# Kernel optimization log

Hardware: AMD Instinct MI355X
Metric: run time of the kernel (lower is better)

## Reference

```python
import jax, jax.numpy as jnp
import numpy as np

NUM_SLOTS = 50
NUM_TAGS = 1 + 2 * NUM_SLOTS  # 'O' + B-/I- per slot = 101
BATCH = 256
SEQ_LEN = 2048


def _build_type_indices():
    # Replicates CRF.build_transitions index construction for a BIO label vocab.
    labels = ['O'] + [p + f's{i}' for i in range(NUM_SLOTS) for p in ('B-', 'I-')]
    m1 = {'O': 0, 'B': 1, 'I': 2}
    m2 = {'O': 0, 'B': 3, 'I': 4}
    t0 = np.zeros((NUM_TAGS, NUM_TAGS), dtype=np.int64)
    t1 = np.zeros((NUM_TAGS, NUM_TAGS), dtype=np.int64)
    for i, li in enumerate(labels):
        for j, lj in enumerate(labels):
            if li != 'O' and li[2:] != lj[2:]:
                t0[i, j], t1[i, j] = m1[li[0]], m2[lj[0]]
            else:
                t0[i, j], t1[i, j] = m1[li[0]], m1[lj[0]]
    return jnp.asarray(t0), jnp.asarray(t1)


def setup_inputs() -> dict:
    key = jax.random.key(0)
    k1, k2, k3, k4, k5, k6 = jax.random.split(key, 6)
    feats = jax.random.normal(k1, (BATCH, SEQ_LEN, NUM_TAGS), dtype=jnp.float32)
    # cdt_transitions is log of the fixed prior table in the original module
    cdt = jnp.log(jnp.array([[0.6, 0.4, 0.001, 0.001, 0.001],
                             [0.3, 0.1, 0.1, 0.5, 0.001],
                             [0.6, 0.1, 0.1, 0.2, 0.001]], dtype=jnp.float32))
    start_transitions = jax.random.normal(k2, (NUM_TAGS,), dtype=jnp.float32)
    stop_transitions = jax.random.normal(k3, (NUM_TAGS,), dtype=jnp.float32)
    # random valid lengths in [S/2, S]; mask[:, :len] = 1
    lengths = jax.random.randint(k4, (BATCH,), SEQ_LEN // 2, SEQ_LEN + 1)
    mask = (jnp.arange(SEQ_LEN)[None, :] < lengths[:, None]).astype(jnp.int32)
    tags = jax.random.randint(k5, (BATCH, SEQ_LEN), 0, NUM_TAGS)
    types0, types1 = _build_type_indices()
    return {
        'feats': feats,
        'cdt_transitions': cdt,
        'start_transitions': start_transitions,
        'stop_transitions': stop_transitions,
        'mask': mask,
        'tags': tags,
        'types0': types0,
        'types1': types1,
    }


def reference(feats, cdt_transitions, start_transitions, stop_transitions,
              mask, tags, types0, types1):
    # build_transitions: gather (num_tags, num_tags) log-transition matrix
    trans = cdt_transitions[types0, types1]  # (T, T)
    B, S, T = feats.shape
    maskb = mask.astype(bool)

    # ---- forward algorithm (log partition) via lax.scan over time ----
    feats_t = jnp.swapaxes(feats, 0, 1)   # (S, B, T)
    mask_t = jnp.swapaxes(maskb, 0, 1)    # (S, B)
    partition0 = feats_t[0] + start_transitions[None, :]  # (B, T)

    def step(partition, xs):
        f, mk = xs  # f: (B, T), mk: (B,)
        # cur_values[b, i, j] = f[b, j] + partition[b, i] + trans[i, j]
        cur = f[:, None, :] + partition[:, :, None] + trans[None, :, :]
        cur_partition = jax.nn.logsumexp(cur, axis=1)  # (B, T)
        new_partition = jnp.where(mk[:, None], cur_partition, partition)
        return new_partition, None

    partition, _ = jax.lax.scan(step, partition0, (feats_t[1:], mask_t[1:]))
    forward_score = jax.nn.logsumexp(partition + stop_transitions[None, :], axis=1)  # (B,)

    # ---- gold path score ----
    mf = maskb.astype(feats.dtype)
    feat_score = jnp.sum(
        jnp.take_along_axis(feats, tags[..., None], axis=2)[..., 0] * mf, axis=1)
    trans_score = jnp.sum(trans[tags[:, :-1], tags[:, 1:]] * mf[:, 1:], axis=1)
    start_score = start_transitions[tags[:, 0]]
    lengths = jnp.sum(mask, axis=1).astype(jnp.int32)  # (B,)
    end_ids = jnp.take_along_axis(tags, (lengths - 1)[:, None], axis=1)[:, 0]
    stop_score = stop_transitions[end_ids]
    gold_score = feat_score + start_score + trans_score + stop_score

    return forward_score - gold_score  # (B,) negative log-likelihood per sequence
```

## Files before the change

kernel.cpp:

```cpp
#include <hip/hip_runtime.h>
#include <math.h>

#define NSLOTS 50
#define T 101
#define SEQ 2048
#define CHUNK 16

template<int CTRL>
__device__ __forceinline__ float dpp_xadd(float v) {
    int x = __builtin_amdgcn_update_dpp(0, __float_as_int(v), CTRL, 0xF, 0xF, true);
    return v + __int_as_float(x);
}

__device__ __forceinline__ float wsum64(float v) {
    v = dpp_xadd<0xB1>(v);
    v = dpp_xadd<0x4E>(v);
    v = dpp_xadd<0x141>(v);
    v = dpp_xadd<0x140>(v);
    v = dpp_xadd<0x142>(v);
    v = dpp_xadd<0x143>(v);
    int s = __builtin_amdgcn_readlane(__float_as_int(v), 63);
    return __int_as_float(s);
}

__device__ __forceinline__ void gl_lds(const float* g, float* lds) {
#if __has_builtin(__builtin_amdgcn_global_load_lds)
    __builtin_amdgcn_global_load_lds((const __attribute__((address_space(1))) void*)g,
        (__attribute__((address_space(3))) void*)lds, 4, 0, 0);
#else
    lds[threadIdx.x & 63] = *g;
#endif
}

__device__ __forceinline__ float frcp(float x) {
#if __has_builtin(__builtin_amdgcn_rcpf)
    return __builtin_amdgcn_rcpf(x);
#else
    return 1.0f / x;
#endif
}
__device__ __forceinline__ float flog2(float x) {
#if __has_builtin(__builtin_amdgcn_log2f)
    return __builtin_amdgcn_log2f(x);
#else
    return log2f(x);
#endif
}

__global__ __launch_bounds__(128, 1) void crf_nll_kernel(
    const float* __restrict__ feats,
    const float* __restrict__ cdt,
    const float* __restrict__ start_t,
    const float* __restrict__ stop_t,
    const int*   __restrict__ mask,
    const int*   __restrict__ tags,
    float*       __restrict__ out)
{
    const int b = blockIdx.x, tid = threadIdx.x;
    const int wave = tid >> 6, l = tid & 63;
    const float* fb = feats + (size_t)b * SEQ * T;
    const int*   mb = mask + (size_t)b * SEQ;
    const int*   tb = tags + (size_t)b * SEQ;

    __shared__ float S[64 * 128];
    __shared__ float res[2];

    float mc = 0.f;
    for (int t = l; t < SEQ; t += 64) mc += (float)mb[t];
    const int len    = (int)(wsum64(mc) + 0.5f);
    const int nsteps = len - 1;
    const int nper   = (nsteps + CHUNK - 1) / CHUNK;
    const int nfull  = nsteps / CHUNK;

    const float actm = (l < NSLOTS) ? 1.f : 0.f;
    const int aB = (2*l+1 <= 100) ? 2*l+1 : 100;
    const int aI = (2*l+2 <= 100) ? 2*l+2 : 100;
    const int s1 = (2*l+1 <= 100) ? 2*l+1 : 0;
    const int s2 = (2*l+2 <= 100) ? 2*l+2 : 0;

    float L[15];
    #pragma unroll
    for (int i = 0; i < 15; ++i) L[i] = cdt[i];
    const float pOO=__expf(L[0]),  pOB=__expf(L[1]),  pOI=__expf(L[2]);
    const float pBO=__expf(L[5]),  pBBs=__expf(L[6]), pBIs=__expf(L[7]),
                pBBd=__expf(L[8]), pBId=__expf(L[9]);
    const float pIO=__expf(L[10]), pIBs=__expf(L[11]), pIIs=__expf(L[12]),
                pIBd=__expf(L[13]), pIId=__expf(L[14]);
    const float dBB=pBBs-pBBd, dIB=pIBs-pIBd, dBI=pBIs-pBId, dII=pIIs-pIId;

    float eB=0.f, eI=0.f, accF=0.f, accL2=0.f;
    float f0B=0,f0I=0,f0O=0,f1B=0,f1I=0,f1O=0;
    float gs = 0.f;

    if (wave == 1) {
        #pragma unroll
        for (int k = 0; k < 2*CHUNK; ++k) {
            const float* row = fb + (size_t)(1 + k) * T;
            float* dst = &S[(size_t)k * 128];
            gl_lds(row + s1, dst);
            gl_lds(row + s2, dst + 64);
        }
    } else {
        float pO0 = fb[0] + start_t[0];
        eB = actm * __expf(fb[aB] + start_t[aB] - pO0);
        eI = actm * __expf(fb[aI] + start_t[aI] - pO0);
        accF = pO0;
    }
    __syncthreads();

    if (wave == 0) {
        f0B = S[l];       f0I = S[64 + l];       f0O = S[50];
        f1B = S[128 + l]; f1I = S[128 + 64 + l]; f1O = S[128 + 50];
    }

#define STEP_BODY(GUARDED)                                                    \
    {                                                                         \
        const int t  = 1 + p * CHUNK + k;                                     \
        const int w2 = ((t + 1) & 63) << 7;     \
        float nB = S[w2 + l], nI = S[w2 + 64 + l], nO = S[w2 + 50];           \
        if (!(GUARDED) || t <= nsteps) {                                      \
            float gB = actm * __expf(f0B - f0O);               \
            float gI = actm * __expf(f0I - f0O);                              \
            float SBs = wsum64(eB);                                           \
            float SIs = wsum64(eI);                                           \
            float uB = __builtin_fmaf(eB,dBB,__builtin_fmaf(eI,dIB,pOB));     \
            float uI = __builtin_fmaf(eB,dBI,__builtin_fmaf(eI,dII,pOI));     \
            float zB = __builtin_fmaf(SIs,pIBd,__builtin_fmaf(SBs,pBBd,uB));  \
            float zI = __builtin_fmaf(SIs,pIId,__builtin_fmaf(SBs,pBId,uI));  \
            float zO = __builtin_fmaf(SIs,pIO, __builtin_fmaf(SBs,pBO,pOO));  \
            float rz = frcp(zO);                                              \
            eB = (gB * zB) * rz;                                              \
            eI = (gI * zI) * rz;                                              \
            accL2 += flog2(zO);                                \
            accF  += f0O;                                      \
        }                                                                     \
        f0B=f1B; f0I=f1I; f0O=f1O; f1B=nB; f1I=nI; f1O=nO;                    \
    }

    for (int p = 0; p < nper; ++p) {
        if (wave == 0) {
            if (p < nfull) {
                #pragma unroll
                for (int k = 0; k < CHUNK; ++k) STEP_BODY(false)
            } else {
                #pragma unroll
                for (int k = 0; k < CHUNK; ++k) STEP_BODY(true)
            }
        } else {
            const int ci = p + 2;
            #pragma unroll
            for (int k = 0; k < CHUNK; ++k) {
                int t = 1 + ci * CHUNK + k;
                t = (t < SEQ) ? t : (SEQ - 1);
                const float* row = fb + (size_t)t * T;
                float* dst = &S[(size_t)((ci * CHUNK + k) & 63) * 128];
                gl_lds(row + s1, dst);
                gl_lds(row + s2, dst + 64);
            }
            if (p < (SEQ / 64)) {
                int t0 = (p << 6) + l;
                if (t0 < len) {
                    int tg = tb[t0];
                    gs += fb[(size_t)t0 * T + tg];
                    if (t0 >= 1) {
                        int i  = tb[t0 - 1];
                        int c1 = (i == 0) ? 0 : ((i & 1) ? 1 : 2);
                        int c2 = (tg == 0) ? 0 : ((tg & 1) ? 1 : 2);
                        int si = (i - 1) >> 1, sj = (tg - 1) >> 1;
                        int t1 = (i != 0 && si != sj) ? ((c2 == 0) ? 0 : c2 + 2) : c2;
                        gs += cdt[c1 * 5 + t1];
                    }
                }
            }
        }
        __syncthreads();
    }
#undef STEP_BODY

    if (wave == 0) {
        float wsum = actm * (eB * __expf(stop_t[aB]) + eI * __expf(stop_t[aI]));
        float tot  = wsum64(wsum) + __expf(stop_t[0]);
        float fwd  = accF + 0.69314718055994530942f * accL2 + __logf(tot);
        if (l == 0) res[0] = fwd;
    } else {
        float gold = wsum64(gs);
        if (l == 0) res[1] = gold + start_t[tb[0]] + stop_t[tb[len - 1]];
    }
    __syncthreads();
    if (tid == 0) out[b] = res[0] - res[1];
}

extern "C" void kernel_launch(void* const* d_in, const int* in_sizes, int n_in,
                              void* d_out, int out_size, void* d_ws, size_t ws_size,
                              hipStream_t stream) {
    const float* feats   = (const float*)d_in[0];
    const float* cdt     = (const float*)d_in[1];
    const float* start_t = (const float*)d_in[2];
    const float* stop_t  = (const float*)d_in[3];
    const int*   mask    = (const int*)d_in[4];
    const int*   tags    = (const int*)d_in[5];
    float* out = (float*)d_out;

    crf_nll_kernel<<<256, 128, 0, stream>>>(feats, cdt, start_t, stop_t, mask, tags, out);
}
```

Measured before the change: 266.9 us.

## Use unnormalized O-state with exponent-only rescaling and add gold-score wave

The forward recurrence now keeps an unnormalized O-state scale xO and renormalizes by a power of two taken from its exponent bits. This removes the per-step reciprocal and log2 from the serial critical path, and the uB/uI partial sums are precomputed for the next step. A third wave computes the gold-path score by reading feature values already staged in LDS instead of issuing separate global gathers, which takes that work off the prefetch wave. The cost is a larger block and extra LDS reads, plus the numerical risk that comes from power-of-two scaling.

```diff
diff --git a/kernel.cpp b/kernel.cpp
--- a/kernel.cpp
+++ b/kernel.cpp
@@ -32,22 +32,7 @@
 #endif
 }
 
-__device__ __forceinline__ float frcp(float x) {
-#if __has_builtin(__builtin_amdgcn_rcpf)
-    return __builtin_amdgcn_rcpf(x);
-#else
-    return 1.0f / x;
-#endif
-}
-__device__ __forceinline__ float flog2(float x) {
-#if __has_builtin(__builtin_amdgcn_log2f)
-    return __builtin_amdgcn_log2f(x);
-#else
-    return log2f(x);
-#endif
-}
-
-__global__ __launch_bounds__(128, 1) void crf_nll_kernel(
+__global__ __launch_bounds__(192, 1) void crf_nll_kernel(
     const float* __restrict__ feats,
     const float* __restrict__ cdt,
     const float* __restrict__ start_t,
@@ -78,17 +63,15 @@
     const int s1 = (2*l+1 <= 100) ? 2*l+1 : 0;
     const int s2 = (2*l+2 <= 100) ? 2*l+2 : 0;
 
-    float L[15];
-    #pragma unroll
-    for (int i = 0; i < 15; ++i) L[i] = cdt[i];
-    const float pOO=__expf(L[0]),  pOB=__expf(L[1]),  pOI=__expf(L[2]);
-    const float pBO=__expf(L[5]),  pBBs=__expf(L[6]), pBIs=__expf(L[7]),
-                pBBd=__expf(L[8]), pBId=__expf(L[9]);
-    const float pIO=__expf(L[10]), pIBs=__expf(L[11]), pIIs=__expf(L[12]),
-                pIBd=__expf(L[13]), pIId=__expf(L[14]);
+    const float pOO=__expf(cdt[0]),  pOB=__expf(cdt[1]),  pOI=__expf(cdt[2]);
+    const float pBO=__expf(cdt[5]),  pBBs=__expf(cdt[6]), pBIs=__expf(cdt[7]),
+                pBBd=__expf(cdt[8]), pBId=__expf(cdt[9]);
+    const float pIO=__expf(cdt[10]), pIBs=__expf(cdt[11]), pIIs=__expf(cdt[12]),
+                pIBd=__expf(cdt[13]), pIId=__expf(cdt[14]);
     const float dBB=pBBs-pBBd, dIB=pIBs-pIBd, dBI=pBIs-pBId, dII=pIIs-pIId;
 
-    float eB=0.f, eI=0.f, accF=0.f, accL2=0.f;
+    float xB=0.f, xI=0.f, xO=1.f, accF=0.f, uB=0.f, uI=0.f, pOOxO=pOO;
+    int accE = 0;
     float f0B=0,f0I=0,f0O=0,f1B=0,f1I=0,f1O=0;
     float gs = 0.f;
 
@@ -100,11 +83,18 @@
             gl_lds(row + s1, dst);
             gl_lds(row + s2, dst + 64);
         }
+    } else if (wave == 0) {
+        float pO0 = fb[0] + start_t[0];
+        xB = actm * __expf(fb[aB] + start_t[aB] - pO0);
+        xI = actm * __expf(fb[aI] + start_t[aI] - pO0);
+        accF = pO0;
+        uB = __builtin_fmaf(xB, dBB, __builtin_fmaf(xI, dIB, pOB));
+        uI = __builtin_fmaf(xB, dBI, __builtin_fmaf(xI, dII, pOI));
     } else {
-        float pO0 = fb[0] + start_t[0];
-        eB = actm * __expf(fb[aB] + start_t[aB] - pO0);
-        eI = actm * __expf(fb[aI] + start_t[aI] - pO0);
-        accF = pO0;
+        if (l == 0) {
+            int tg0 = tb[0];
+            gs = fb[tg0] + start_t[tg0];
+        }
     }
     __syncthreads();
 
@@ -113,28 +103,29 @@
         f1B = S[128 + l]; f1I = S[128 + 64 + l]; f1O = S[128 + 50];
     }
 
-#define STEP_BODY(GUARDED)                                                    \
-    {                                                                         \
-        const int t  = 1 + p * CHUNK + k;                                     \
-        const int w2 = ((t + 1) & 63) << 7;     \
-        float nB = S[w2 + l], nI = S[w2 + 64 + l], nO = S[w2 + 50];           \
-        if (!(GUARDED) || t <= nsteps) {                                      \
-            float gB = actm * __expf(f0B - f0O);               \
-            float gI = actm * __expf(f0I - f0O);                              \
-            float SBs = wsum64(eB);                                           \
-            float SIs = wsum64(eI);                                           \
-            float uB = __builtin_fmaf(eB,dBB,__builtin_fmaf(eI,dIB,pOB));     \
-            float uI = __builtin_fmaf(eB,dBI,__builtin_fmaf(eI,dII,pOI));     \
-            float zB = __builtin_fmaf(SIs,pIBd,__builtin_fmaf(SBs,pBBd,uB));  \
-            float zI = __builtin_fmaf(SIs,pIId,__builtin_fmaf(SBs,pBId,uI));  \
-            float zO = __builtin_fmaf(SIs,pIO, __builtin_fmaf(SBs,pBO,pOO));  \
-            float rz = frcp(zO);                                              \
-            eB = (gB * zB) * rz;                                              \
-            eI = (gI * zI) * rz;                                              \
-            accL2 += flog2(zO);                                \
-            accF  += f0O;                                      \
-        }                                                                     \
-        f0B=f1B; f0I=f1I; f0O=f1O; f1B=nB; f1I=nI; f1O=nO;                    \
+#define STEP_BODY(GUARDED)                                                     \
+    {                                                                          \
+        const int t  = 1 + p * CHUNK + k;                                      \
+        const int w2 = ((t + 1) & 63) << 7;              \
+        float nB = S[w2 + l], nI = S[w2 + 64 + l], nO = S[w2 + 50];            \
+        if (!(GUARDED) || t <= nsteps) {                                       \
+            float gB = actm * __expf(f0B - f0O);                \
+            float gI = actm * __expf(f0I - f0O);                               \
+            int   ke = ((__float_as_int(xO) >> 23) & 0xFF) - 127;              \
+            float r  = __int_as_float((127 - ke) << 23);     \
+            accE += ke;                                                        \
+            float XB = wsum64(xB);                                             \
+            float XI = wsum64(xI);                                             \
+            float NOr = __builtin_fmaf(XI,pIO, __builtin_fmaf(XB,pBO, pOOxO));  \
+            float NB  = gB * __builtin_fmaf(XI,pIBd, __builtin_fmaf(XB,pBBd, uB)); \
+            float NI  = gI * __builtin_fmaf(XI,pIId, __builtin_fmaf(XB,pBId, uI)); \
+            xB = NB * r; xI = NI * r; xO = NOr * r;                            \
+            pOOxO = pOO * xO;                          \
+            uB = __builtin_fmaf(xB, dBB, __builtin_fmaf(xI, dIB, pOB * xO));   \
+            uI = __builtin_fmaf(xB, dBI, __builtin_fmaf(xI, dII, pOI * xO));   \
+            accF += f0O;                                                       \
+        }                                                                      \
+        f0B=f1B; f0I=f1I; f0O=f1O; f1B=nB; f1I=nI; f1O=nO;                     \
     }
 
     for (int p = 0; p < nper; ++p) {
@@ -146,7 +137,7 @@
                 #pragma unroll
                 for (int k = 0; k < CHUNK; ++k) STEP_BODY(true)
             }
-        } else {
+        } else if (wave == 1) {
             const int ci = p + 2;
             #pragma unroll
             for (int k = 0; k < CHUNK; ++k) {
@@ -157,19 +148,18 @@
                 gl_lds(row + s1, dst);
                 gl_lds(row + s2, dst + 64);
             }
-            if (p < (SEQ / 64)) {
-                int t0 = (p << 6) + l;
-                if (t0 < len) {
-                    int tg = tb[t0];
-                    gs += fb[(size_t)t0 * T + tg];
-                    if (t0 >= 1) {
-                        int i  = tb[t0 - 1];
-                        int c1 = (i == 0) ? 0 : ((i & 1) ? 1 : 2);
-                        int c2 = (tg == 0) ? 0 : ((tg & 1) ? 1 : 2);
-                        int si = (i - 1) >> 1, sj = (tg - 1) >> 1;
-                        int t1 = (i != 0 && si != sj) ? ((c2 == 0) ? 0 : c2 + 2) : c2;
-                        gs += cdt[c1 * 5 + t1];
-                    }
+        } else {
+            if (p >= 1 && l < CHUNK) {
+                int t = 1 + (p - 1) * CHUNK + l;
+                if (t <= nsteps) {
+                    int tg = tb[t], tp = tb[t - 1];
+                    int c1 = (tp == 0) ? 0 : ((tp & 1) ? 1 : 2);
+                    int c2 = (tg == 0) ? 0 : ((tg & 1) ? 1 : 2);
+                    int si = (tp - 1) >> 1, sj = (tg - 1) >> 1;
+                    int t1 = (tp != 0 && si != sj) ? ((c2 == 0) ? 0 : c2 + 2) : c2;
+                    gs += cdt[c1 * 5 + t1];
+                    int idx = (tg == 0) ? 50 : ((tg & 1) ? ((tg - 1) >> 1) : (64 + ((tg - 2) >> 1)));
+                    gs += S[(((t - 1) & 63) << 7) + idx];
                 }
             }
         }
@@ -178,13 +168,26 @@
 #undef STEP_BODY
 
     if (wave == 0) {
-        float wsum = actm * (eB * __expf(stop_t[aB]) + eI * __expf(stop_t[aI]));
-        float tot  = wsum64(wsum) + __expf(stop_t[0]);
-        float fwd  = accF + 0.69314718055994530942f * accL2 + __logf(tot);
+        float W = actm * (xB * __expf(stop_t[aB]) + xI * __expf(stop_t[aI]));
+        float tot = wsum64(W) + xO * __expf(stop_t[0]);
+        float fwd = accF + 0.69314718055994530942f * (float)accE + __logf(tot);
         if (l == 0) res[0] = fwd;
-    } else {
+    } else if (wave == 2) {
+        if (l < CHUNK) {
+            int t = 1 + (nper - 1) * CHUNK + l;
+            if (t >= 1 && t <= nsteps) {
+                int tg = tb[t], tp = tb[t - 1];
+                int c1 = (tp == 0) ? 0 : ((tp & 1) ? 1 : 2);
+                int c2 = (tg == 0) ? 0 : ((tg & 1) ? 1 : 2);
+                int si = (tp - 1) >> 1, sj = (tg - 1) >> 1;
+                int t1 = (tp != 0 && si != sj) ? ((c2 == 0) ? 0 : c2 + 2) : c2;
+                gs += cdt[c1 * 5 + t1];
+                int idx = (tg == 0) ? 50 : ((tg & 1) ? ((tg - 1) >> 1) : (64 + ((tg - 2) >> 1)));
+                gs += S[(((t - 1) & 63) << 7) + idx];
+            }
+        }
         float gold = wsum64(gs);
-        if (l == 0) res[1] = gold + start_t[tb[0]] + stop_t[tb[len - 1]];
+        if (l == 0) res[1] = gold + stop_t[tb[len - 1]];
     }
     __syncthreads();
     if (tid == 0) out[b] = res[0] - res[1];
@@ -201,5 +204,5 @@
     const int*   tags    = (const int*)d_in[5];
     float* out = (float*)d_out;
 
-    crf_nll_kernel<<<256, 128, 0, stream>>>(feats, cdt, start_t, stop_t, mask, tags, out);
-}
+    crf_nll_kernel<<<256, 192, 0, stream>>>(feats, cdt, start_t, stop_t, mask, tags, out);
+}
```

New measurement: 246.7 us. 7.6% less time.
